# Performance work log

Hardware: AMD Instinct MI355X
Metric: run time of the kernel (lower is better)

## Reference

```python
import jax, jax.numpy as jnp
import numpy as np

N = 100000   # nodes
E = 600000   # edges
G = 512      # graphs in batch
EPS = 1e-5   # LayerNorm eps
IN_DIM = 60 + 2 + 12  # dyn feats*frames + dims + st embedding
H = 128


def setup_inputs() -> dict:
    key = jax.random.key(0)
    ks = jax.random.split(key, 32)
    inp = {
        "x": jax.random.normal(ks[0], (N, 60), jnp.float32),
        "xdims": jax.random.uniform(ks[1], (N, 2), jnp.float32),
        "xsttype": jax.random.randint(ks[2], (N,), 0, 256, jnp.int32),
        "edge_index": jax.random.randint(ks[3], (2, E), 0, N, jnp.int32),
        "batch": jnp.sort(jax.random.randint(ks[4], (N,), 0, G, jnp.int32)),
        "emb": jax.random.normal(ks[5], (256, 12), jnp.float32),
    }
    def lin(k, i, o):
        s = 1.0 / np.sqrt(i)
        return jax.random.uniform(k, (i, o), jnp.float32, -s, s)
    dims = [IN_DIM, H, H]
    for l in range(2):
        i, o = dims[l], dims[l + 1]
        inp[f"Wl{l}"] = lin(ks[6 + 4 * l], i, o)   # lin_l: applied to aggregated neighbors
        inp[f"bl{l}"] = jnp.zeros((o,), jnp.float32)
        inp[f"Wr{l}"] = lin(ks[7 + 4 * l], i, o)   # lin_r: applied to root (no bias, PyG SAGEConv)
        inp[f"g{l}"] = jnp.ones((o,), jnp.float32)   # LayerNorm gamma
        inp[f"bn{l}"] = jnp.zeros((o,), jnp.float32)  # LayerNorm beta
    ld = [2 * H, 50, 50, 10]
    for l in range(3):
        inp[f"Wf{l}"] = lin(ks[20 + l], ld[l], ld[l + 1])
        inp[f"bf{l}"] = jnp.zeros((ld[l + 1],), jnp.float32)
    return inp


def _layer_norm(h, g, b):
    mu = jnp.mean(h, axis=-1, keepdims=True)
    var = jnp.mean(jnp.square(h - mu), axis=-1, keepdims=True)
    return (h - mu) * jax.lax.rsqrt(var + EPS) * g + b


def reference(x, xdims, xsttype, edge_index, batch, emb,
              Wl0, bl0, Wr0, g0, bn0,
              Wl1, bl1, Wr1, g1, bn1,
              Wf0, bf0, Wf1, bf1, Wf2, bf2):
    # node feature assembly: [N, 60+2+12]
    h = jnp.concatenate([x, xdims, emb[xsttype]], axis=1)

    src, dst = edge_index[0], edge_index[1]
    deg = jax.ops.segment_sum(jnp.ones((E,), h.dtype), dst, num_segments=N)
    inv_deg = (1.0 / jnp.maximum(deg, 1.0))[:, None]

    for Wl, bl, Wr, g, bn in ((Wl0, bl0, Wr0, g0, bn0), (Wl1, bl1, Wr1, g1, bn1)):
        # SAGEConv (mean aggr): out = lin_l(mean_j x_j) + lin_r(x_i)
        agg = jax.ops.segment_sum(h[src], dst, num_segments=N) * inv_deg
        h = agg @ Wl + bl + h @ Wr
        h = jax.nn.relu(_layer_norm(h, g, bn))  # dropout inactive (eval)

    # global mean / max pooling over graphs
    cnt = jax.ops.segment_sum(jnp.ones((N,), h.dtype), batch, num_segments=G)
    xmean = jax.ops.segment_sum(h, batch, num_segments=G) / jnp.maximum(cnt, 1.0)[:, None]
    xmax = jax.ops.segment_max(h, batch, num_segments=G)
    z = jnp.concatenate([xmean, xmax], axis=1)  # [G, 2H]

    for Wf, bf in ((Wf0, bf0), (Wf1, bf1), (Wf2, bf2)):
        z = jax.nn.relu(z @ Wf + bf)  # Linear + ReLU + Dropout(eval)
    return z
```

## Files before the change

### kernel.cpp

```cpp
#include <hip/hip_runtime.h>

#define NN 100000
#define NP 100096
#define NT (NP / 32)
#define EE 600000
#define GG 512
#define LN_EPS 1e-5f

typedef __attribute__((ext_vector_type(8))) __bf16 bf16x8;
typedef __attribute__((ext_vector_type(4))) float f32x4;

__device__ __forceinline__ unsigned short f2bf(float f) {
    unsigned int u = __float_as_uint(f);
    u = (u + 0x7fffu + ((u >> 16) & 1u)) >> 16;
    return (unsigned short)u;
}
__device__ __forceinline__ unsigned int pack2(float a, float b) {
    return (unsigned int)f2bf(a) | ((unsigned int)f2bf(b) << 16);
}
__device__ __forceinline__ void acc8(float* s, uint4 v) {
    s[0] += __uint_as_float(v.x << 16);
    s[1] += __uint_as_float(v.x & 0xffff0000u);
    s[2] += __uint_as_float(v.y << 16);
    s[3] += __uint_as_float(v.y & 0xffff0000u);
    s[4] += __uint_as_float(v.z << 16);
    s[5] += __uint_as_float(v.z & 0xffff0000u);
    s[6] += __uint_as_float(v.w << 16);
    s[7] += __uint_as_float(v.w & 0xffff0000u);
}

#define PREP_A (NP * 10)
#define PREP_W0 (128 * 160)
#define PREP_W1 (128 * 256)
#define PREP_TOT (PREP_A + PREP_W0 + PREP_W1 + EE)

__global__ __launch_bounds__(256) void prep_kernel(
    const float* __restrict__ x, const float* __restrict__ xdims,
    const int* __restrict__ stt, const float* __restrict__ emb,
    const int* __restrict__ ei,
    const float* __restrict__ Wl0, const float* __restrict__ Wr0,
    const float* __restrict__ Wl1, const float* __restrict__ Wr1,
    unsigned short* __restrict__ H0r,
    unsigned short* __restrict__ Wt0, unsigned short* __restrict__ Wt1,
    int* __restrict__ deg)
{
    int idx = blockIdx.x * 256 + threadIdx.x;
    if (idx < PREP_A) {
        int node = idx / 10;
        int c8 = (idx - node * 10) * 8;
        unsigned short vals[8];
        if (node < NN) {
            int st = stt[node];
            #pragma unroll
            for (int i = 0; i < 8; ++i) {
                int f = c8 + i;
                float v = 0.f;
                if (f < 60)      v = x[node * 60 + f];
                else if (f < 62) v = xdims[node * 2 + (f - 60)];
                else if (f < 74) v = emb[st * 12 + (f - 62)];
                vals[i] = f2bf(v);
            }
        } else {
            #pragma unroll
            for (int i = 0; i < 8; ++i) vals[i] = 0;
        }
        uint4 o;
        o.x = (unsigned)vals[0] | ((unsigned)vals[1] << 16);
        o.y = (unsigned)vals[2] | ((unsigned)vals[3] << 16);
        o.z = (unsigned)vals[4] | ((unsigned)vals[5] << 16);
        o.w = (unsigned)vals[6] | ((unsigned)vals[7] << 16);
        *(uint4*)(H0r + (size_t)node * 80 + c8) = o;
    } else if (idx < PREP_A + PREP_W0) {
        int j = idx - PREP_A;
        int n = j / 160, k = j - n * 160;
        float v = 0.f;
        if (k < 74)                  v = Wl0[k * 128 + n];
        else if (k >= 80 && k < 154) v = Wr0[(k - 80) * 128 + n];
        Wt0[(size_t)n * 160 + k] = f2bf(v);
    } else if (idx < PREP_A + PREP_W0 + PREP_W1) {
        int j = idx - PREP_A - PREP_W0;
        int n = j >> 8, k = j & 255;
        float v = (k < 128) ? Wl1[k * 128 + n] : Wr1[(k - 128) * 128 + n];
        Wt1[(size_t)n * 256 + k] = f2bf(v);
    } else if (idx < PREP_TOT) {
        int e = idx - PREP_A - PREP_W0 - PREP_W1;
        atomicAdd(&deg[ei[EE + e]], 1);
    }
}

__global__ __launch_bounds__(256) void scan1_kernel(
    const int* __restrict__ deg, int* __restrict__ offs, int* __restrict__ bsum)
{
    __shared__ int ts[256];
    int t = threadIdx.x;
    int base = blockIdx.x * 2048 + t * 8;
    int d[8];
    if (base + 8 <= NN) {
        int4 a = *(const int4*)&deg[base];
        int4 b = *(const int4*)&deg[base + 4];
        d[0]=a.x; d[1]=a.y; d[2]=a.z; d[3]=a.w;
        d[4]=b.x; d[5]=b.y; d[6]=b.z; d[7]=b.w;
    } else {
        #pragma unroll
        for (int i = 0; i < 8; ++i) d[i] = (base + i < NN) ? deg[base + i] : 0;
    }
    int e[8]; int run = 0;
    #pragma unroll
    for (int i = 0; i < 8; ++i) { e[i] = run; run += d[i]; }
    ts[t] = run;
    int tot = run;
    __syncthreads();
    for (int off = 1; off < 256; off <<= 1) {
        int u = (t >= off) ? ts[t - off] : 0;
        __syncthreads();
        ts[t] += u;
        __syncthreads();
    }
    int pre = ts[t] - tot;
    #pragma unroll
    for (int i = 0; i < 8; ++i) if (base + i < NN) offs[base + i] = e[i] + pre;
    if (t == 255) bsum[blockIdx.x] = ts[255];
}

__global__ void scan2_kernel(int* __restrict__ bsum, int nb)
{
    int t = threadIdx.x;
    int v = (t < nb) ? bsum[t] : 0;
    int inc = v;
    for (int off = 1; off < 64; off <<= 1) {
        int u = __shfl_up(inc, off, 64);
        if (t >= off) inc += u;
    }
    if (t < nb) bsum[t] = inc - v;
}

__global__ __launch_bounds__(256) void fill_csr_kernel(
    const int* __restrict__ ei, int* __restrict__ cur,
    const int* __restrict__ offs, const int* __restrict__ bsum,
    int* __restrict__ csr)
{
    int e = blockIdx.x * 256 + threadIdx.x;
    if (e >= EE) return;
    int d = ei[EE + e];
    int p = offs[d] + bsum[d >> 11] + atomicAdd(&cur[d], 1);
    csr[p] = ei[e];
}

__global__ __launch_bounds__(256) void agg0_kernel(
    const unsigned short* __restrict__ H0r, unsigned short* __restrict__ A0g,
    const int* __restrict__ csr, const int* __restrict__ offs,
    const int* __restrict__ bsum, const int* __restrict__ deg)
{
    int node = blockIdx.x * 16 + (threadIdx.x >> 4);
    int lane = threadIdx.x & 15;
    if (node >= NP || lane >= 10) return;
    int d = 0, st = 0;
    if (node < NN) { d = deg[node]; st = offs[node] + bsum[node >> 11]; }
    float iv = 1.0f / (float)(d > 1 ? d : 1);
    float s[8];
    #pragma unroll
    for (int i = 0; i < 8; ++i) s[i] = 0.f;
    int e = 0;
    for (; e + 4 <= d; e += 4) {
        int i0 = csr[st + e],     i1 = csr[st + e + 1];
        int i2 = csr[st + e + 2], i3 = csr[st + e + 3];
        uint4 v0 = *(const uint4*)(H0r + (size_t)i0 * 80 + lane * 8);
        uint4 v1 = *(const uint4*)(H0r + (size_t)i1 * 80 + lane * 8);
        uint4 v2 = *(const uint4*)(H0r + (size_t)i2 * 80 + lane * 8);
        uint4 v3 = *(const uint4*)(H0r + (size_t)i3 * 80 + lane * 8);
        acc8(s, v0); acc8(s, v1); acc8(s, v2); acc8(s, v3);
    }
    for (; e < d; ++e) {
        int i0 = csr[st + e];
        uint4 v0 = *(const uint4*)(H0r + (size_t)i0 * 80 + lane * 8);
        acc8(s, v0);
    }
    uint4 o;
    o.x = pack2(s[0] * iv, s[1] * iv);
    o.y = pack2(s[2] * iv, s[3] * iv);
    o.z = pack2(s[4] * iv, s[5] * iv);
    o.w = pack2(s[6] * iv, s[7] * iv);
    *(uint4*)(A0g + (size_t)node * 80 + lane * 8) = o;
}

__global__ __launch_bounds__(256) void agg1_kernel(
    const unsigned short* __restrict__ H1, unsigned short* __restrict__ A1g,
    const int* __restrict__ csr, const int* __restrict__ offs,
    const int* __restrict__ bsum, const int* __restrict__ deg)
{
    int node = blockIdx.x * 16 + (threadIdx.x >> 4);
    int lane = threadIdx.x & 15;
    if (node >= NP) return;
    int d = 0, st = 0;
    if (node < NN) { d = deg[node]; st = offs[node] + bsum[node >> 11]; }
    float iv = 1.0f / (float)(d > 1 ? d : 1);
    float s[8];
    #pragma unroll
    for (int i = 0; i < 8; ++i) s[i] = 0.f;
    int e = 0;
    for (; e + 4 <= d; e += 4) {
        int i0 = csr[st + e],     i1 = csr[st + e + 1];
        int i2 = csr[st + e + 2], i3 = csr[st + e + 3];
        uint4 v0 = *(const uint4*)(H1 + (size_t)i0 * 128 + lane * 8);
        uint4 v1 = *(const uint4*)(H1 + (size_t)i1 * 128 + lane * 8);
        uint4 v2 = *(const uint4*)(H1 + (size_t)i2 * 128 + lane * 8);
        uint4 v3 = *(const uint4*)(H1 + (size_t)i3 * 128 + lane * 8);
        acc8(s, v0); acc8(s, v1); acc8(s, v2); acc8(s, v3);
    }
    for (; e < d; ++e) {
        int i0 = csr[st + e];
        uint4 v0 = *(const uint4*)(H1 + (size_t)i0 * 128 + lane * 8);
        acc8(s, v0);
    }
    uint4 o;
    o.x = pack2(s[0] * iv, s[1] * iv);
    o.y = pack2(s[2] * iv, s[3] * iv);
    o.z = pack2(s[4] * iv, s[5] * iv);
    o.w = pack2(s[6] * iv, s[7] * iv);
    *(uint4*)(A1g + (size_t)node * 128 + lane * 8) = o;
}

template<int K, bool POOL>
__global__ __launch_bounds__(256, 4) void gemm_kernel(
    const unsigned short* __restrict__ Ag,
    const unsigned short* __restrict__ Hr,
    const unsigned short* __restrict__ Wt,
    const float* __restrict__ bias, const float* __restrict__ gamma,
    const float* __restrict__ beta,
    unsigned short* __restrict__ outH,
    const int* __restrict__ batch,
    float* __restrict__ psum, int* __restrict__ pmax)
{
    constexpr int KT = K / 32, AS = K + 8, CPR = K / 8, CPRh = CPR / 2, KH = K / 2;
    constexpr int SMEM = (32 * AS * 2 > 32 * 128 * 4) ? 32 * AS * 2 : 32 * 128 * 4;
    __shared__ __align__(16) char smem[SMEM];
    unsigned short* Asm = (unsigned short*)smem;
    float* Hs = (float*)smem;
    __shared__ __align__(16) float sP[32 * 4];
    __shared__ __align__(16) float qP[32 * 4];
    __shared__ int bS[POOL ? 32 : 1];

    const int tid = threadIdx.x;
    const int n0 = blockIdx.x * 32;

    if (POOL && tid < 32) {
        int gn = n0 + tid;
        bS[tid] = (gn < NN) ? batch[gn] : -1;
    }
    for (int i = tid; i < 32 * CPR; i += 256) {
        int node = i / CPR, c = i - node * CPR;
        size_t gn = (size_t)(n0 + node);
        const unsigned short* src = (c < CPRh)
            ? (Ag + gn * KH + c * 8)
            : (Hr + gn * KH + (c - CPRh) * 8);
        uint4 v = *(const uint4*)src;
        *(uint4*)(Asm + node * AS + c * 8) = v;
    }

    const int l = tid & 63, w = tid >> 6;
    const int g = l >> 4, c0 = l & 15;
    float bia[2], gam[2], bet[2];
    #pragma unroll
    for (int j = 0; j < 2; ++j) {
        int col = (2 * w + j) * 16 + c0;
        bia[j] = bias[col]; gam[j] = gamma[col]; bet[j] = beta[col];
    }
    const unsigned short* bp0 = Wt + (size_t)((2 * w + 0) * 16 + c0) * K + g * 8;
    const unsigned short* bp1 = Wt + (size_t)((2 * w + 1) * 16 + c0) * K + g * 8;
    const unsigned short* ar0 = Asm + (0 * 16 + c0) * AS + g * 8;
    const unsigned short* ar1 = Asm + (1 * 16 + c0) * AS + g * 8;
    __syncthreads();

    f32x4 acc[2][2];
    acc[0][0] = (f32x4){0.f,0.f,0.f,0.f}; acc[0][1] = (f32x4){0.f,0.f,0.f,0.f};
    acc[1][0] = (f32x4){0.f,0.f,0.f,0.f}; acc[1][1] = (f32x4){0.f,0.f,0.f,0.f};

    #pragma unroll
    for (int kt = 0; kt < KT; ++kt) {
        bf16x8 b0 = *(const bf16x8*)(bp0 + kt * 32);
        bf16x8 b1 = *(const bf16x8*)(bp1 + kt * 32);
        bf16x8 a0 = *(const bf16x8*)(ar0 + kt * 32);
        bf16x8 a1 = *(const bf16x8*)(ar1 + kt * 32);
        acc[0][0] = __builtin_amdgcn_mfma_f32_16x16x32_bf16(a0, b0, acc[0][0], 0, 0, 0);
        acc[0][1] = __builtin_amdgcn_mfma_f32_16x16x32_bf16(a0, b1, acc[0][1], 0, 0, 0);
        acc[1][0] = __builtin_amdgcn_mfma_f32_16x16x32_bf16(a1, b0, acc[1][0], 0, 0, 0);
        acc[1][1] = __builtin_amdgcn_mfma_f32_16x16x32_bf16(a1, b1, acc[1][1], 0, 0, 0);
    }

    #pragma unroll
    for (int m = 0; m < 2; ++m) {
        #pragma unroll
        for (int r = 0; r < 4; ++r) {
            float h0v = acc[m][0][r] + bia[0];
            float h1v = acc[m][1][r] + bia[1];
            float s = h0v + h1v, q = h0v * h0v + h1v * h1v;
            #pragma unroll
            for (int mm = 1; mm < 16; mm <<= 1) {
                s += __shfl_xor(s, mm, 64);
                q += __shfl_xor(q, mm, 64);
            }
            if (c0 == 0) {
                int node = m * 16 + g * 4 + r;
                sP[node * 4 + w] = s;
                qP[node * 4 + w] = q;
            }
        }
    }
    __syncthreads();

    #pragma unroll
    for (int m = 0; m < 2; ++m) {
        #pragma unroll
        for (int r = 0; r < 4; ++r) {
            int node = m * 16 + g * 4 + r;
            float4 sv = *(const float4*)&sP[node * 4];
            float4 qv = *(const float4*)&qP[node * 4];
            float s = (sv.x + sv.y) + (sv.z + sv.w);
            float q = (qv.x + qv.y) + (qv.z + qv.w);
            float mu   = s * (1.f / 128.f);
            float var  = q * (1.f / 128.f) - mu * mu;
            float rinv = rsqrtf(var + LN_EPS);
            float h0v = acc[m][0][r] + bia[0];
            float h1v = acc[m][1][r] + bia[1];
            float v0 = fmaxf(0.f, (h0v - mu) * rinv * gam[0] + bet[0]);
            float v1 = fmaxf(0.f, (h1v - mu) * rinv * gam[1] + bet[1]);
            if (POOL) {
                Hs[node * 128 + (2 * w) * 16 + c0]     = v0;
                Hs[node * 128 + (2 * w + 1) * 16 + c0] = v1;
            } else {
                size_t gn = (size_t)(n0 + node);
                outH[gn * 128 + (2 * w) * 16 + c0]     = f2bf(v0);
                outH[gn * 128 + (2 * w + 1) * 16 + c0] = f2bf(v1);
            }
        }
    }
    if (!POOL) return;
    __syncthreads();

    if (tid < 128) {
        int j = tid;
        int curg = -1; float s = 0.f, m = 0.f;
        #pragma unroll 4
        for (int n = 0; n < 32; ++n) {
            int gb = bS[n];
            if (gb < 0) break;
            if (gb != curg) {
                if (curg >= 0) {
                    atomicAdd(&psum[curg * 128 + j], s);
                    atomicMax(&pmax[curg * 128 + j], __float_as_int(m));
                }
                curg = gb; s = 0.f; m = 0.f;
            }
            float v = Hs[n * 128 + j];
            s += v; m = fmaxf(m, v);
        }
        if (curg >= 0) {
            atomicAdd(&psum[curg * 128 + j], s);
            atomicMax(&pmax[curg * 128 + j], __float_as_int(m));
        }
    }
}

__device__ __forceinline__ int lbound(const int* a, int n, int v) {
    int lo = 0, hi = n;
    while (lo < hi) { int mid = (lo + hi) >> 1; if (a[mid] < v) lo = mid + 1; else hi = mid; }
    return lo;
}

__global__ __launch_bounds__(64) void mlp_kernel(
    const float* __restrict__ psum, const int* __restrict__ pmax,
    const int* __restrict__ batch,
    const float* __restrict__ Wf0, const float* __restrict__ bf0,
    const float* __restrict__ Wf1, const float* __restrict__ bf1,
    const float* __restrict__ Wf2, const float* __restrict__ bf2,
    float* __restrict__ out)
{
    __shared__ float z[256];
    __shared__ float t1[50];
    __shared__ float t2[50];
    __shared__ int cS;
    int g = blockIdx.x, t = threadIdx.x;
    if (t == 0) cS = lbound(batch, NN, g + 1) - lbound(batch, NN, g);
    __syncthreads();
    int c = cS;
    float ic = 1.0f / (float)(c > 1 ? c : 1);
    for (int j = t; j < 128; j += 64) {
        z[j]       = psum[g * 128 + j] * ic;
        z[128 + j] = __int_as_float(pmax[g * 128 + j]);
    }
    __syncthreads();
    if (t < 50) {
        float a = bf0[t];
        for (int k = 0; k < 256; ++k) a = fmaf(z[k], Wf0[k * 50 + t], a);
        t1[t] = fmaxf(a, 0.0f);
    }
    __syncthreads();
    if (t < 50) {
        float a = bf1[t];
        for (int k = 0; k < 50; ++k) a = fmaf(t1[k], Wf1[k * 50 + t], a);
        t2[t] = fmaxf(a, 0.0f);
    }
    __syncthreads();
    if (t < 10) {
        float a = bf2[t];
        for (int k = 0; k < 50; ++k) a = fmaf(t2[k], Wf2[k * 10 + t], a);
        out[g * 10 + t] = fmaxf(a, 0.0f);
    }
}

extern "C" void kernel_launch(void* const* d_in, const int* in_sizes, int n_in,
                              void* d_out, int out_size, void* d_ws, size_t ws_size,
                              hipStream_t stream)
{
    const float* x     = (const float*)d_in[0];
    const float* xdims = (const float*)d_in[1];
    const int*   stt   = (const int*)d_in[2];
    const int*   ei    = (const int*)d_in[3];
    const int*   batch = (const int*)d_in[4];
    const float* emb   = (const float*)d_in[5];
    const float* Wl0   = (const float*)d_in[6];
    const float* bl0   = (const float*)d_in[7];
    const float* Wr0   = (const float*)d_in[8];
    const float* g0    = (const float*)d_in[9];
    const float* bn0   = (const float*)d_in[10];
    const float* Wl1   = (const float*)d_in[11];
    const float* bl1   = (const float*)d_in[12];
    const float* Wr1   = (const float*)d_in[13];
    const float* g1    = (const float*)d_in[14];
    const float* bn1   = (const float*)d_in[15];
    const float* Wf0   = (const float*)d_in[16];
    const float* bf0   = (const float*)d_in[17];
    const float* Wf1   = (const float*)d_in[18];
    const float* bf1   = (const float*)d_in[19];
    const float* Wf2   = (const float*)d_in[20];
    const float* bf2   = (const float*)d_in[21];

    char* w = (char*)d_ws;
    unsigned short* H0r = (unsigned short*)w; w += (size_t)NP * 80 * 2;
    unsigned short* A0g = (unsigned short*)w; w += (size_t)NP * 80 * 2;
    unsigned short* H1  = (unsigned short*)w; w += (size_t)NP * 128 * 2;
    unsigned short* A1g = (unsigned short*)w; w += (size_t)NP * 128 * 2;
    unsigned short* Wt0 = (unsigned short*)w; w += (size_t)128 * 160 * 2;
    unsigned short* Wt1 = (unsigned short*)w; w += (size_t)128 * 256 * 2;
    int*   csr    = (int*)w;   w += (size_t)EE * 4;
    int*   offs   = (int*)w;   w += (size_t)NN * 4;
    int*   bsum   = (int*)w;   w += 1024;
    char* zbeg = w;
    int*   deg  = (int*)w;   w += (size_t)NP * 4;
    int*   cur  = (int*)w;   w += (size_t)NN * 4;
    float* psum = (float*)w; w += (size_t)GG * 128 * 4;
    int*   pmax = (int*)w;   w += (size_t)GG * 128 * 4;
    size_t zsz = (size_t)(w - zbeg);

    hipMemsetAsync(zbeg, 0, zsz, stream);

    prep_kernel<<<(PREP_TOT + 255) / 256, 256, 0, stream>>>(
        x, xdims, stt, emb, ei, Wl0, Wr0, Wl1, Wr1, H0r, Wt0, Wt1, deg);

    int nb = (NN + 2047) / 2048;
    scan1_kernel<<<nb, 256, 0, stream>>>(deg, offs, bsum);
    scan2_kernel<<<1, 64, 0, stream>>>(bsum, nb);
    fill_csr_kernel<<<(EE + 255) / 256, 256, 0, stream>>>(ei, cur, offs, bsum, csr);

    agg0_kernel<<<NP / 16, 256, 0, stream>>>(H0r, A0g, csr, offs, bsum, deg);
    gemm_kernel<160, false><<<NT, 256, 0, stream>>>(
        A0g, H0r, Wt0, bl0, g0, bn0, H1, nullptr, nullptr, nullptr);
    agg1_kernel<<<NP / 16, 256, 0, stream>>>(H1, A1g, csr, offs, bsum, deg);
    gemm_kernel<256, true><<<NT, 256, 0, stream>>>(
        A1g, H1, Wt1, bl1, g1, bn1, nullptr, batch, psum, pmax);

    mlp_kernel<<<GG, 64, 0, stream>>>(psum, pmax, batch, Wf0, bf0, Wf1, bf1, Wf2, bf2,
                                      (float*)d_out);
}
```

Baseline: 310.4 us.

## Fuse neighbor mean aggregation into SAGE GEMM tile loads and count graphs in pooling

Removes the separate agg0/agg1 kernels. Each GEMM block now gathers and averages neighbor rows for its 32 nodes directly into shared memory, next to the root features. This removes the write and re-read of the intermediate aggregated arrays and two kernel launches. Per-graph node counts are also accumulated with atomics during pooling instead of binary searches in the MLP kernel. The cost is that the gather latency now sits inside the GEMM blocks, and occupancy is limited by the GEMM's launch bounds.

Result: faster. 283.5 us (-8.7%).

```diff
diff --git a/kernel.cpp b/kernel.cpp
--- a/kernel.cpp
+++ b/kernel.cpp
@@ -146,92 +146,19 @@
     csr[p] = ei[e];
 }
 
-__global__ __launch_bounds__(256) void agg0_kernel(
-    const unsigned short* __restrict__ H0r, unsigned short* __restrict__ A0g,
-    const int* __restrict__ csr, const int* __restrict__ offs,
-    const int* __restrict__ bsum, const int* __restrict__ deg)
-{
-    int node = blockIdx.x * 16 + (threadIdx.x >> 4);
-    int lane = threadIdx.x & 15;
-    if (node >= NP || lane >= 10) return;
-    int d = 0, st = 0;
-    if (node < NN) { d = deg[node]; st = offs[node] + bsum[node >> 11]; }
-    float iv = 1.0f / (float)(d > 1 ? d : 1);
-    float s[8];
-    #pragma unroll
-    for (int i = 0; i < 8; ++i) s[i] = 0.f;
-    int e = 0;
-    for (; e + 4 <= d; e += 4) {
-        int i0 = csr[st + e],     i1 = csr[st + e + 1];
-        int i2 = csr[st + e + 2], i3 = csr[st + e + 3];
-        uint4 v0 = *(const uint4*)(H0r + (size_t)i0 * 80 + lane * 8);
-        uint4 v1 = *(const uint4*)(H0r + (size_t)i1 * 80 + lane * 8);
-        uint4 v2 = *(const uint4*)(H0r + (size_t)i2 * 80 + lane * 8);
-        uint4 v3 = *(const uint4*)(H0r + (size_t)i3 * 80 + lane * 8);
-        acc8(s, v0); acc8(s, v1); acc8(s, v2); acc8(s, v3);
-    }
-    for (; e < d; ++e) {
-        int i0 = csr[st + e];
-        uint4 v0 = *(const uint4*)(H0r + (size_t)i0 * 80 + lane * 8);
-        acc8(s, v0);
-    }
-    uint4 o;
-    o.x = pack2(s[0] * iv, s[1] * iv);
-    o.y = pack2(s[2] * iv, s[3] * iv);
-    o.z = pack2(s[4] * iv, s[5] * iv);
-    o.w = pack2(s[6] * iv, s[7] * iv);
-    *(uint4*)(A0g + (size_t)node * 80 + lane * 8) = o;
-}
-
-__global__ __launch_bounds__(256) void agg1_kernel(
-    const unsigned short* __restrict__ H1, unsigned short* __restrict__ A1g,
-    const int* __restrict__ csr, const int* __restrict__ offs,
-    const int* __restrict__ bsum, const int* __restrict__ deg)
-{
-    int node = blockIdx.x * 16 + (threadIdx.x >> 4);
-    int lane = threadIdx.x & 15;
-    if (node >= NP) return;
-    int d = 0, st = 0;
-    if (node < NN) { d = deg[node]; st = offs[node] + bsum[node >> 11]; }
-    float iv = 1.0f / (float)(d > 1 ? d : 1);
-    float s[8];
-    #pragma unroll
-    for (int i = 0; i < 8; ++i) s[i] = 0.f;
-    int e = 0;
-    for (; e + 4 <= d; e += 4) {
-        int i0 = csr[st + e],     i1 = csr[st + e + 1];
-        int i2 = csr[st + e + 2], i3 = csr[st + e + 3];
-        uint4 v0 = *(const uint4*)(H1 + (size_t)i0 * 128 + lane * 8);
-        uint4 v1 = *(const uint4*)(H1 + (size_t)i1 * 128 + lane * 8);
-        uint4 v2 = *(const uint4*)(H1 + (size_t)i2 * 128 + lane * 8);
-        uint4 v3 = *(const uint4*)(H1 + (size_t)i3 * 128 + lane * 8);
-        acc8(s, v0); acc8(s, v1); acc8(s, v2); acc8(s, v3);
-    }
-    for (; e < d; ++e) {
-        int i0 = csr[st + e];
-        uint4 v0 = *(const uint4*)(H1 + (size_t)i0 * 128 + lane * 8);
-        acc8(s, v0);
-    }
-    uint4 o;
-    o.x = pack2(s[0] * iv, s[1] * iv);
-    o.y = pack2(s[2] * iv, s[3] * iv);
-    o.z = pack2(s[4] * iv, s[5] * iv);
-    o.w = pack2(s[6] * iv, s[7] * iv);
-    *(uint4*)(A1g + (size_t)node * 128 + lane * 8) = o;
-}
-
 template<int K, bool POOL>
 __global__ __launch_bounds__(256, 4) void gemm_kernel(
-    const unsigned short* __restrict__ Ag,
     const unsigned short* __restrict__ Hr,
     const unsigned short* __restrict__ Wt,
     const float* __restrict__ bias, const float* __restrict__ gamma,
     const float* __restrict__ beta,
     unsigned short* __restrict__ outH,
     const int* __restrict__ batch,
-    float* __restrict__ psum, int* __restrict__ pmax)
-{
-    constexpr int KT = K / 32, AS = K + 8, CPR = K / 8, CPRh = CPR / 2, KH = K / 2;
+    float* __restrict__ psum, int* __restrict__ pmax, int* __restrict__ gcnt,
+    const int* __restrict__ csr, const int* __restrict__ offs,
+    const int* __restrict__ bsum, const int* __restrict__ deg)
+{
+    constexpr int KT = K / 32, AS = K + 8, KH = K / 2, CH = KH / 8;
     constexpr int SMEM = (32 * AS * 2 > 32 * 128 * 4) ? 32 * AS * 2 : 32 * 128 * 4;
     __shared__ __align__(16) char smem[SMEM];
     unsigned short* Asm = (unsigned short*)smem;
@@ -242,33 +169,64 @@
 
     const int tid = threadIdx.x;
     const int n0 = blockIdx.x * 32;
+    const int l = tid & 63, w = tid >> 6;
+    const int fg = l >> 4, c0 = l & 15;
 
     if (POOL && tid < 32) {
         int gn = n0 + tid;
         bS[tid] = (gn < NN) ? batch[gn] : -1;
     }
-    for (int i = tid; i < 32 * CPR; i += 256) {
-        int node = i / CPR, c = i - node * CPR;
-        size_t gn = (size_t)(n0 + node);
-        const unsigned short* src = (c < CPRh)
-            ? (Ag + gn * KH + c * 8)
-            : (Hr + gn * KH + (c - CPRh) * 8);
-        uint4 v = *(const uint4*)src;
-        *(uint4*)(Asm + node * AS + c * 8) = v;
-    }
-
-    const int l = tid & 63, w = tid >> 6;
-    const int g = l >> 4, c0 = l & 15;
     float bia[2], gam[2], bet[2];
     #pragma unroll
     for (int j = 0; j < 2; ++j) {
         int col = (2 * w + j) * 16 + c0;
         bia[j] = bias[col]; gam[j] = gamma[col]; bet[j] = beta[col];
     }
-    const unsigned short* bp0 = Wt + (size_t)((2 * w + 0) * 16 + c0) * K + g * 8;
-    const unsigned short* bp1 = Wt + (size_t)((2 * w + 1) * 16 + c0) * K + g * 8;
-    const unsigned short* ar0 = Asm + (0 * 16 + c0) * AS + g * 8;
-    const unsigned short* ar1 = Asm + (1 * 16 + c0) * AS + g * 8;
+    const unsigned short* bp0 = Wt + (size_t)((2 * w + 0) * 16 + c0) * K + fg * 8;
+    const unsigned short* bp1 = Wt + (size_t)((2 * w + 1) * 16 + c0) * K + fg * 8;
+
+    {
+        const int ln = tid & 15, nl = tid >> 4;
+        #pragma unroll
+        for (int half = 0; half < 2; ++half) {
+            int node = half * 16 + nl;
+            int gn = n0 + node;
+            if (ln < CH) {
+                uint4 rv = *(const uint4*)(Hr + (size_t)gn * KH + ln * 8);
+                int d = 0, st = 0;
+                if (gn < NN) { d = deg[gn]; st = offs[gn] + bsum[gn >> 11]; }
+                float iv = 1.0f / (float)(d > 1 ? d : 1);
+                float s[8];
+                #pragma unroll
+                for (int i = 0; i < 8; ++i) s[i] = 0.f;
+                int e = 0;
+                for (; e + 4 <= d; e += 4) {
+                    int i0 = csr[st + e],     i1 = csr[st + e + 1];
+                    int i2 = csr[st + e + 2], i3 = csr[st + e + 3];
+                    uint4 v0 = *(const uint4*)(Hr + (size_t)i0 * KH + ln * 8);
+                    uint4 v1 = *(const uint4*)(Hr + (size_t)i1 * KH + ln * 8);
+                    uint4 v2 = *(const uint4*)(Hr + (size_t)i2 * KH + ln * 8);
+                    uint4 v3 = *(const uint4*)(Hr + (size_t)i3 * KH + ln * 8);
+                    acc8(s, v0); acc8(s, v1); acc8(s, v2); acc8(s, v3);
+                }
+                for (; e < d; ++e) {
+                    int i0 = csr[st + e];
+                    uint4 v0 = *(const uint4*)(Hr + (size_t)i0 * KH + ln * 8);
+                    acc8(s, v0);
+                }
+                uint4 o;
+                o.x = pack2(s[0] * iv, s[1] * iv);
+                o.y = pack2(s[2] * iv, s[3] * iv);
+                o.z = pack2(s[4] * iv, s[5] * iv);
+                o.w = pack2(s[6] * iv, s[7] * iv);
+                *(uint4*)(Asm + node * AS + ln * 8) = o;
+                *(uint4*)(Asm + node * AS + KH + ln * 8) = rv;
+            }
+        }
+    }
+
+    const unsigned short* ar0 = Asm + (0 * 16 + c0) * AS + fg * 8;
+    const unsigned short* ar1 = Asm + (1 * 16 + c0) * AS + fg * 8;
     __syncthreads();
 
     f32x4 acc[2][2];
@@ -300,7 +258,7 @@
                 q += __shfl_xor(q, mm, 64);
             }
             if (c0 == 0) {
-                int node = m * 16 + g * 4 + r;
+                int node = m * 16 + fg * 4 + r;
                 sP[node * 4 + w] = s;
                 qP[node * 4 + w] = q;
             }
@@ -312,7 +270,7 @@
     for (int m = 0; m < 2; ++m) {
         #pragma unroll
         for (int r = 0; r < 4; ++r) {
-            int node = m * 16 + g * 4 + r;
+            int node = m * 16 + fg * 4 + r;
             float4 sv = *(const float4*)&sP[node * 4];
             float4 qv = *(const float4*)&qP[node * 4];
             float s = (sv.x + sv.y) + (sv.z + sv.w);
@@ -339,7 +297,7 @@
 
     if (tid < 128) {
         int j = tid;
-        int curg = -1; float s = 0.f, m = 0.f;
+        int curg = -1; float s = 0.f, m = 0.f; int rl = 0;
         #pragma unroll 4
         for (int n = 0; n < 32; ++n) {
             int gb = bS[n];
@@ -348,28 +306,25 @@
                 if (curg >= 0) {
                     atomicAdd(&psum[curg * 128 + j], s);
                     atomicMax(&pmax[curg * 128 + j], __float_as_int(m));
+                    if (j == 0) atomicAdd(&gcnt[curg], rl);
                 }
-                curg = gb; s = 0.f; m = 0.f;
+                curg = gb; s = 0.f; m = 0.f; rl = 0;
             }
             float v = Hs[n * 128 + j];
             s += v; m = fmaxf(m, v);
+            rl += 1;
         }
         if (curg >= 0) {
             atomicAdd(&psum[curg * 128 + j], s);
             atomicMax(&pmax[curg * 128 + j], __float_as_int(m));
-        }
-    }
-}
-
-__device__ __forceinline__ int lbound(const int* a, int n, int v) {
-    int lo = 0, hi = n;
-    while (lo < hi) { int mid = (lo + hi) >> 1; if (a[mid] < v) lo = mid + 1; else hi = mid; }
-    return lo;
+            if (j == 0) atomicAdd(&gcnt[curg], rl);
+        }
+    }
 }
 
 __global__ __launch_bounds__(64) void mlp_kernel(
     const float* __restrict__ psum, const int* __restrict__ pmax,
-    const int* __restrict__ batch,
+    const int* __restrict__ gcnt,
     const float* __restrict__ Wf0, const float* __restrict__ bf0,
     const float* __restrict__ Wf1, const float* __restrict__ bf1,
     const float* __restrict__ Wf2, const float* __restrict__ bf2,
@@ -378,11 +333,8 @@
     __shared__ float z[256];
     __shared__ float t1[50];
     __shared__ float t2[50];
-    __shared__ int cS;
     int g = blockIdx.x, t = threadIdx.x;
-    if (t == 0) cS = lbound(batch, NN, g + 1) - lbound(batch, NN, g);
-    __syncthreads();
-    int c = cS;
+    int c = gcnt[g];
     float ic = 1.0f / (float)(c > 1 ? c : 1);
     for (int j = t; j < 128; j += 64) {
         z[j]       = psum[g * 128 + j] * ic;
@@ -437,9 +389,7 @@
 
     char* w = (char*)d_ws;
     unsigned short* H0r = (unsigned short*)w; w += (size_t)NP * 80 * 2;
-    unsigned short* A0g = (unsigned short*)w; w += (size_t)NP * 80 * 2;
     unsigned short* H1  = (unsigned short*)w; w += (size_t)NP * 128 * 2;
-    unsigned short* A1g = (unsigned short*)w; w += (size_t)NP * 128 * 2;
     unsigned short* Wt0 = (unsigned short*)w; w += (size_t)128 * 160 * 2;
     unsigned short* Wt1 = (unsigned short*)w; w += (size_t)128 * 256 * 2;
     int*   csr    = (int*)w;   w += (size_t)EE * 4;
@@ -450,6 +400,7 @@
     int*   cur  = (int*)w;   w += (size_t)NN * 4;
     float* psum = (float*)w; w += (size_t)GG * 128 * 4;
     int*   pmax = (int*)w;   w += (size_t)GG * 128 * 4;
+    int*   gcnt = (int*)w;   w += (size_t)GG * 4;
     size_t zsz = (size_t)(w - zbeg);
 
     hipMemsetAsync(zbeg, 0, zsz, stream);
@@ -462,13 +413,13 @@
     scan2_kernel<<<1, 64, 0, stream>>>(bsum, nb);
     fill_csr_kernel<<<(EE + 255) / 256, 256, 0, stream>>>(ei, cur, offs, bsum, csr);
 
-    agg0_kernel<<<NP / 16, 256, 0, stream>>>(H0r, A0g, csr, offs, bsum, deg);
     gemm_kernel<160, false><<<NT, 256, 0, stream>>>(
-        A0g, H0r, Wt0, bl0, g0, bn0, H1, nullptr, nullptr, nullptr);
-    agg1_kernel<<<NP / 16, 256, 0, stream>>>(H1, A1g, csr, offs, bsum, deg);
+        H0r, Wt0, bl0, g0, bn0, H1, nullptr, nullptr, nullptr, nullptr,
+        csr, offs, bsum, deg);
     gemm_kernel<256, true><<<NT, 256, 0, stream>>>(
-        A1g, H1, Wt1, bl1, g1, bn1, nullptr, batch, psum, pmax);
-
-    mlp_kernel<<<GG, 64, 0, stream>>>(psum, pmax, batch, Wf0, bf0, Wf1, bf1, Wf2, bf2,
+        H1, Wt1, bl1, g1, bn1, nullptr, batch, psum, pmax, gcnt,
+        csr, offs, bsum, deg);
+
+    mlp_kernel<<<GG, 64, 0, stream>>>(psum, pmax, gcnt, Wf0, bf0, Wf1, bf1, Wf2, bf2,
                                       (float*)d_out);
 }
```
